# Kernel optimization log

Hardware: AMD Instinct MI355X
Metric: run time of the kernel (lower is better)

## Reference

```python
import jax, jax.numpy as jnp
import numpy as np

B, T, D = 1, 2048, 2048
HQ, HKV = 32, 8
DH = D // HQ          # 64
NREP = HQ // HKV      # 4


def _apply_rope(x, cos, sin):
    # x: (B, T, H, DH); cos/sin: (T, DH//2). Complex multiply on interleaved pairs:
    # (x0 + i*x1) * (c + i*s) -> (x0*c - x1*s, x0*s + x1*c)
    b, t, h, d = x.shape
    xr = x.reshape(b, t, h, d // 2, 2)
    x0, x1 = xr[..., 0], xr[..., 1]
    c = cos[:t][None, :, None, :]
    s = sin[:t][None, :, None, :]
    o0 = x0 * c - x1 * s
    o1 = x0 * s + x1 * c
    return jnp.stack([o0, o1], axis=-1).reshape(b, t, h, d)


def setup_inputs() -> dict:
    key = jax.random.key(0)
    ks = jax.random.split(key, 6)
    w = 0.02
    x = jax.random.normal(ks[0], (B, T, D), dtype=jnp.float32)
    Wq = jax.random.normal(ks[1], (HQ * DH, D), dtype=jnp.float32) * w
    Wk = jax.random.normal(ks[2], (HKV * DH, D), dtype=jnp.float32) * w
    Wv = jax.random.normal(ks[3], (HKV * DH, D), dtype=jnp.float32) * w
    Wo = jax.random.normal(ks[4], (D, HQ * DH), dtype=jnp.float32) * w
    # standard RoPE frequencies, theta = 10000
    inv_freq = 1.0 / (10000.0 ** (np.arange(0, DH, 2, dtype=np.float32) / DH))
    angles = np.arange(T, dtype=np.float32)[:, None] * inv_freq[None, :]  # (T, DH//2)
    rope_cos = jnp.asarray(np.cos(angles))
    rope_sin = jnp.asarray(np.sin(angles))
    mask = jnp.tril(jnp.ones((T, T), dtype=bool))  # causal
    return {"x": x, "Wq": Wq, "Wk": Wk, "Wv": Wv, "Wo": Wo,
            "rope_cos": rope_cos, "rope_sin": rope_sin, "mask": mask}


def reference(x, Wq, Wk, Wv, Wo, rope_cos, rope_sin, mask):
    b, t, d = x.shape
    q = (x @ Wq.T).reshape(b, t, HQ, DH)
    k = (x @ Wk.T).reshape(b, t, HKV, DH)
    v = (x @ Wv.T).reshape(b, t, HKV, DH)
    q = _apply_rope(q, rope_cos, rope_sin)
    k = _apply_rope(k, rope_cos, rope_sin)
    # GQA: head index = kv_head * NREP + rep (matches torch expand+reshape order)
    qg = q.reshape(b, t, HKV, NREP, DH)
    scale = jnp.sqrt(jnp.float32(DH))
    # scores: (B, HKV, NREP, T, S) without materializing expanded K
    scores = jnp.einsum('bthrd,bshd->bhrts', qg, k) / scale
    scores = jnp.where(mask[None, None, None, :t, :t], scores, -jnp.inf)
    attn = jax.nn.softmax(scores, axis=-1)
    out = jnp.einsum('bhrts,bshd->bthrd', attn, v)  # (B, T, HKV, NREP, DH)
    out = out.reshape(b, t, HQ * DH)
    return out @ Wo.T
```

## Files before the change

kernel.cpp:

```cpp
#include <hip/hip_runtime.h>
#include <math.h>
#include <stdint.h>

static constexpr int T   = 2048;
static constexpr int D   = 2048;
static constexpr int HQ  = 32;
static constexpr int HKV = 8;
static constexpr int DH  = 64;
static constexpr int DKV = HKV * DH;
static constexpr int NQKV = D + 2 * DKV;

typedef float f32x4 __attribute__((ext_vector_type(4)));
typedef __bf16 bf16x8 __attribute__((ext_vector_type(8)));
typedef __bf16 bf16x2 __attribute__((ext_vector_type(2)));
typedef unsigned short u16x8 __attribute__((ext_vector_type(8)));
typedef unsigned short u16x4 __attribute__((ext_vector_type(4)));

__device__ __forceinline__ unsigned short f2bf(float f) {
  union { float f; unsigned u; } v; v.f = f;
  unsigned u = v.u;
  return (unsigned short)((u + 0x7FFFu + ((u >> 16) & 1u)) >> 16);
}
__device__ __forceinline__ float bf2f(unsigned short b) {
  union { unsigned u; float f; } v; v.u = ((unsigned)b) << 16;
  return v.f;
}
__device__ __forceinline__ unsigned pk2bf(float a, float b) {
#if __has_builtin(__builtin_amdgcn_cvt_pk_bf16_f32)
  bf16x2 r = __builtin_amdgcn_cvt_pk_bf16_f32(a, b);
  return __builtin_bit_cast(unsigned, r);
#else
  return (unsigned)f2bf(a) | ((unsigned)f2bf(b) << 16);
#endif
}
__device__ __forceinline__ float fexp2(float x) {
#if __has_builtin(__builtin_amdgcn_exp2f)
  return __builtin_amdgcn_exp2f(x);
#else
  return exp2f(x);
#endif
}
__device__ __forceinline__ float frcp(float x) {
#if __has_builtin(__builtin_amdgcn_rcpf)
  return __builtin_amdgcn_rcpf(x);
#else
  return 1.0f / x;
#endif
}
__device__ __forceinline__ f32x4 mfma16(u16x8 a, u16x8 b, f32x4 c) {
  return __builtin_amdgcn_mfma_f32_16x16x32_bf16(
      __builtin_bit_cast(bf16x8, a), __builtin_bit_cast(bf16x8, b), c, 0, 0, 0);
}
__device__ __forceinline__ void gld16(const unsigned short* g, unsigned short* l) {
  __builtin_amdgcn_global_load_lds(
      (const __attribute__((address_space(1))) unsigned*)g,
      (__attribute__((address_space(3))) unsigned*)l, 16, 0, 0);
}

__global__ __launch_bounds__(256) void cvt_all(const float* __restrict__ x,
                                               const float* __restrict__ Wq,
                                               const float* __restrict__ Wk,
                                               const float* __restrict__ Wv,
                                               const float* __restrict__ Wo,
                                               unsigned short* __restrict__ xb,
                                               unsigned short* __restrict__ wqkv,
                                               unsigned short* __restrict__ wob) {
  int b = blockIdx.x;
  const float* src;
  unsigned short* dst;
  if (b < 2048)      { src = x;  dst = xb; }
  else if (b < 4096) { src = Wq; dst = wqkv;                          b -= 2048; }
  else if (b < 4608) { src = Wk; dst = wqkv + (size_t)D * D;          b -= 4096; }
  else if (b < 5120) { src = Wv; dst = wqkv + (size_t)(D + DKV) * D;  b -= 4608; }
  else               { src = Wo; dst = wob;                           b -= 5120; }
  size_t i = ((size_t)b * 256 + threadIdx.x) * 8;
  float4 a = *(const float4*)(src + i);
  float4 c = *(const float4*)(src + i + 4);
  uint4 r = {pk2bf(a.x, a.y), pk2bf(a.z, a.w), pk2bf(c.x, c.y), pk2bf(c.z, c.w)};
  *(uint4*)(dst + i) = r;
}

template <bool OUT_BF16>
__global__ __launch_bounds__(256) void gemm_bt_bf16(const unsigned short* __restrict__ A,
                                                    const unsigned short* __restrict__ Bt,
                                                    void* __restrict__ Cv,
                                                    int N, int K) {
  __shared__ alignas(16) unsigned short As[64 * 128];
  __shared__ alignas(16) unsigned short Bs[128 * 128];

  const int bn = blockIdx.x * 128, bm = blockIdx.y * 64;
  const int tid = threadIdx.x, w = tid >> 6, lane = tid & 63;
  const int c = lane & 15, quad = lane >> 4;

  const int r4 = lane >> 4, ch = lane & 15;
  const unsigned short* aRow = A + (size_t)(bm + w * 16 + r4) * K;
  const unsigned short* bRow = Bt + (size_t)(bn + w * 32 + r4) * K;
  unsigned short* AsW = As + (w * 16) * 128;
  unsigned short* BsW = Bs + (w * 32) * 128;

  f32x4 acc[4][2] = {};

  for (int k0 = 0; k0 < K; k0 += 128) {
#pragma unroll
    for (int j = 0; j < 4; j++) {
      const int sch = ch ^ ((j * 4 + r4) & 15);
      gld16(aRow + (size_t)(j * 4) * K + k0 + sch * 8, AsW + j * 4 * 128);
    }
#pragma unroll
    for (int j = 0; j < 8; j++) {
      const int sch = ch ^ ((j * 4 + r4) & 15);
      gld16(bRow + (size_t)(j * 4) * K + k0 + sch * 8, BsW + j * 4 * 128);
    }
    __syncthreads();

#pragma unroll
    for (int ks = 0; ks < 4; ks++) {
      const int slot = (ks * 4 + quad) ^ c;
      u16x8 a[4], b[2];
#pragma unroll
      for (int mi = 0; mi < 4; mi++)
        a[mi] = *(const u16x8*)&As[(mi * 16 + c) * 128 + slot * 8];
#pragma unroll
      for (int ni = 0; ni < 2; ni++)
        b[ni] = *(const u16x8*)&Bs[(w * 32 + ni * 16 + c) * 128 + slot * 8];
#pragma unroll
      for (int mi = 0; mi < 4; mi++)
#pragma unroll
        for (int ni = 0; ni < 2; ni++)
          acc[mi][ni] = mfma16(a[mi], b[ni], acc[mi][ni]);
    }
    __syncthreads();
  }

#pragma unroll
  for (int mi = 0; mi < 4; mi++)
#pragma unroll
    for (int ni = 0; ni < 2; ni++)
#pragma unroll
      for (int r = 0; r < 4; r++) {
        size_t row = (size_t)(bm + mi * 16 + quad * 4 + r);
        size_t col = (size_t)(bn + w * 32 + ni * 16 + c);
        if (OUT_BF16)
          ((unsigned short*)Cv)[row * N + col] = f2bf(acc[mi][ni][r]);
        else
          ((float*)Cv)[row * N + col] = acc[mi][ni][r];
      }
}

__global__ __launch_bounds__(256) void rope_tv(unsigned short* __restrict__ QKV,
                                               const float* __restrict__ cosb,
                                               const float* __restrict__ sinb,
                                               unsigned short* __restrict__ VT) {
  const int QP = T * HQ * (DH / 2);
  if (blockIdx.x < 10240) {
    int idx = blockIdx.x * 256 + threadIdx.x;
    unsigned short* p;
    int t, i;
    float sc;
    if (idx < QP) {
      t = idx / (HQ * DH / 2);
      int rem = idx - t * (HQ * DH / 2);
      i = rem & 31;
      p = QKV + (size_t)t * NQKV + rem * 2;
      sc = 0.125f * 1.44269504088896340736f;
    } else {
      int j = idx - QP;
      t = j / (HKV * DH / 2);
      int rem = j - t * (HKV * DH / 2);
      i = rem & 31;
      p = QKV + (size_t)t * NQKV + D + rem * 2;
      sc = 1.0f;
    }
    float x0 = bf2f(p[0]), x1 = bf2f(p[1]);
    float cs = cosb[t * 32 + i], sn = sinb[t * 32 + i];
    *(unsigned*)p = pk2bf((x0 * cs - x1 * sn) * sc, (x0 * sn + x1 * cs) * sc);
  } else {
    __shared__ unsigned short Ts[64][65];
    const int bid = blockIdx.x - 10240;
    const int tb = bid & 31, db = bid >> 5;
    const int tid = threadIdx.x;
    const int r = tid >> 2, c0 = (tid & 3) * 16;
    const unsigned short* src = QKV + (size_t)(tb * 64 + r) * NQKV + (D + DKV) + db * 64 + c0;
    *(u16x8*)&Ts[r][c0]     = *(const u16x8*)src;
    *(u16x8*)&Ts[r][c0 + 8] = *(const u16x8*)(src + 8);
    __syncthreads();
    u16x8 a, b;
#pragma unroll
    for (int j = 0; j < 8; j++) a[j] = Ts[c0 + j][r];
#pragma unroll
    for (int j = 0; j < 8; j++) b[j] = Ts[c0 + 8 + j][r];
    unsigned short* dst = VT + (size_t)(db * 64 + r) * T + tb * 64 + c0;
    *(u16x8*)dst = a;
    *(u16x8*)(dst + 8) = b;
  }
}

__global__ __launch_bounds__(256) void attn_kernel(const unsigned short* __restrict__ QKV,
                                                   const unsigned short* __restrict__ VT,
                                                   unsigned short* __restrict__ Ob) {
  const int kh = blockIdx.x;
  const int NQT = T / 16;
  const int tid = threadIdx.x, w = tid >> 6, lane = tid & 63;
  const int c = lane & 15, quad = lane >> 4;
  const int h = kh * 4 + w;

  __shared__ alignas(16) unsigned short Kt[64 * 64];
  __shared__ alignas(16) unsigned short Vt[64 * 64];
  __shared__ alignas(16) unsigned short Pb[4 * 16 * 72];

  unsigned short* PbW = Pb + w * 16 * 72;

  const int srow = lane >> 3;
  const int sch  = (lane & 7) ^ srow;
  const unsigned short* kgBase = QKV + D + (size_t)(w * 16 + srow) * NQKV + kh * DH + sch * 8;
  const unsigned short* vgBase = VT + (size_t)(kh * DH + w * 16 + srow) * T + sch * 8;
  unsigned short* KtW = Kt + (w * 16) * 64;
  unsigned short* VtW = Vt + (w * 16) * 64;

#pragma unroll 1
  for (int pass = 0; pass < 2; pass++) {
    const int qt = pass ? (NQT - 1 - (int)blockIdx.y) : (int)blockIdx.y;
    const int qbase = qt * 16;

    u16x8 qf[2];
    {
      const unsigned short* qp = QKV + (size_t)(qbase + c) * NQKV + h * DH + quad * 8;
      qf[0] = *(const u16x8*)qp;
      qf[1] = *(const u16x8*)(qp + 32);
    }

    f32x4 o[4] = {};
    float m = -INFINITY, l = 0.f;

    const int nFull = qt >> 2;
    for (int st = 0; st <= nFull; st++) {
      __syncthreads();
#pragma unroll
      for (int j = 0; j < 2; j++) {
        gld16(kgBase + ((size_t)st * 64 + (size_t)j * 8) * NQKV, KtW + j * 8 * 64);
        gld16(vgBase + (size_t)j * 8 * T + st * 64, VtW + j * 8 * 64);
      }
      __syncthreads();

      f32x4 sacc[4] = {};
#pragma unroll
      for (int ks = 0; ks < 2; ks++) {
#pragma unroll
        for (int ni = 0; ni < 4; ni++) {
          const int slot = (ks * 4 + quad) ^ (c & 7);
          u16x8 kf = *(const u16x8*)&Kt[(ni * 16 + c) * 64 + slot * 8];
          sacc[ni] = mfma16(kf, qf[ks], sacc[ni]);
        }
      }

      if (st == nFull) {
        const int qrow = qbase + c;
#pragma unroll
        for (int ni = 0; ni < 4; ni++)
#pragma unroll
          for (int r = 0; r < 4; r++) {
            int key = st * 64 + ni * 16 + quad * 4 + r;
            if (key > qrow) sacc[ni][r] = -INFINITY;
          }
      }

      float tmax = sacc[0][0];
#pragma unroll
      for (int ni = 0; ni < 4; ni++)
#pragma unroll
        for (int r = 0; r < 4; r++) tmax = fmaxf(tmax, sacc[ni][r]);
      tmax = fmaxf(tmax, __shfl_xor(tmax, 16, 64));
      tmax = fmaxf(tmax, __shfl_xor(tmax, 32, 64));
      float mnew = fmaxf(m, tmax);
      float alpha = fexp2(m - mnew);
      m = mnew;

      float psum = 0.f;
#pragma unroll
      for (int ni = 0; ni < 4; ni++) {
        float p0 = fexp2(sacc[ni][0] - mnew);
        float p1 = fexp2(sacc[ni][1] - mnew);
        float p2 = fexp2(sacc[ni][2] - mnew);
        float p3 = fexp2(sacc[ni][3] - mnew);
        psum += (p0 + p1) + (p2 + p3);
        uint2 pr = {pk2bf(p0, p1), pk2bf(p2, p3)};
        *(uint2*)&PbW[c * 72 + ni * 16 + quad * 4] = pr;
      }
      psum += __shfl_xor(psum, 16, 64);
      psum += __shfl_xor(psum, 32, 64);
      l = l * alpha + psum;

      float aR[4];
#pragma unroll
      for (int r = 0; r < 4; r++) aR[r] = __shfl(alpha, quad * 4 + r, 64);
#pragma unroll
      for (int ni = 0; ni < 4; ni++)
#pragma unroll
        for (int r = 0; r < 4; r++) o[ni][r] *= aR[r];

#pragma unroll
      for (int ks = 0; ks < 2; ks++) {
        u16x8 pf = *(const u16x8*)&PbW[c * 72 + ks * 32 + quad * 8];
#pragma unroll
        for (int ni = 0; ni < 4; ni++) {
          const int slot = (ks * 4 + quad) ^ (c & 7);
          u16x8 vf = *(const u16x8*)&Vt[(ni * 16 + c) * 64 + slot * 8];
          o[ni] = mfma16(pf, vf, o[ni]);
        }
      }
    }

    float lR[4];
#pragma unroll
    for (int r = 0; r < 4; r++) lR[r] = frcp(__shfl(l, quad * 4 + r, 64));
#pragma unroll
    for (int ni = 0; ni < 4; ni++)
#pragma unroll
      for (int r = 0; r < 4; r++) {
        size_t row = (size_t)(qbase + quad * 4 + r);
        size_t col = (size_t)(h * DH + ni * 16 + c);
        Ob[row * D + col] = f2bf(o[ni][r] * lR[r]);
      }
  }
}

extern "C" void kernel_launch(void* const* d_in, const int* in_sizes, int n_in,
                              void* d_out, int out_size, void* d_ws, size_t ws_size,
                              hipStream_t stream) {
  const float* x  = (const float*)d_in[0];
  const float* Wq = (const float*)d_in[1];
  const float* Wk = (const float*)d_in[2];
  const float* Wv = (const float*)d_in[3];
  const float* Wo = (const float*)d_in[4];
  const float* rc = (const float*)d_in[5];
  const float* rs = (const float*)d_in[6];
  float* out = (float*)d_out;

  char* ws = (char*)d_ws;
  unsigned short* xb   = (unsigned short*)(ws);
  unsigned short* wqkv = (unsigned short*)(ws + (size_t)(8u  << 20));
  unsigned short* wob  = (unsigned short*)(ws + (size_t)(20u << 20));
  unsigned short* qkvb = (unsigned short*)(ws + (size_t)(28u << 20));
  unsigned short* Ab   = xb;
  unsigned short* VT   = wqkv;

  cvt_all<<<dim3(7168), 256, 0, stream>>>(x, Wq, Wk, Wv, Wo, xb, wqkv, wob);

  gemm_bt_bf16<true><<<dim3(NQKV / 128, T / 64), 256, 0, stream>>>(xb, wqkv, qkvb, NQKV, D);

  rope_tv<<<dim3(10240 + 256), 256, 0, stream>>>(qkvb, rc, rs, VT);

  attn_kernel<<<dim3(HKV, T / 32), 256, 0, stream>>>(qkvb, VT, Ab);

  gemm_bt_bf16<false><<<dim3(D / 128, T / 64), 256, 0, stream>>>(Ab, wob, out, D, D);
}
```

Before: 228.3 us.

## Double-buffer GEMM and attention tiles, one query tile per attention block

The GEMM drops from one 128-wide K tile to two ping-pong 64-wide shared-memory buffers. The next tile's async global-to-LDS load is issued before computing on the current one, leaving one barrier per iteration. The attention kernel gets the same K/V double buffering. It also drops the paired forward/reverse query-tile passes in favour of one query tile per block, launched in reverse order to put the heavy tiles first. This aims to hide load latency and raise parallelism, but it loses the causal load pairing and adds LDS use.

After: 233.2 us. 2.1% more time.

```diff
diff --git a/kernel.cpp b/kernel.cpp
--- a/kernel.cpp
+++ b/kernel.cpp
@@ -85,51 +85,54 @@
                                                     const unsigned short* __restrict__ Bt,
                                                     void* __restrict__ Cv,
                                                     int N, int K) {
-  __shared__ alignas(16) unsigned short As[64 * 128];
-  __shared__ alignas(16) unsigned short Bs[128 * 128];
+  __shared__ alignas(16) unsigned short As[2][64 * 64];
+  __shared__ alignas(16) unsigned short Bs[2][128 * 64];
 
   const int bn = blockIdx.x * 128, bm = blockIdx.y * 64;
   const int tid = threadIdx.x, w = tid >> 6, lane = tid & 63;
   const int c = lane & 15, quad = lane >> 4;
 
-  const int r4 = lane >> 4, ch = lane & 15;
-  const unsigned short* aRow = A + (size_t)(bm + w * 16 + r4) * K;
-  const unsigned short* bRow = Bt + (size_t)(bn + w * 32 + r4) * K;
-  unsigned short* AsW = As + (w * 16) * 128;
-  unsigned short* BsW = Bs + (w * 32) * 128;
+  const int sr8 = lane >> 3;
+  const int sc8 = (lane & 7) ^ sr8;
+  const unsigned short* aRow = A + (size_t)(bm + w * 16 + sr8) * K + sc8 * 8;
+  const unsigned short* bRow = Bt + (size_t)(bn + w * 32 + sr8) * K + sc8 * 8;
 
   f32x4 acc[4][2] = {};
 
-  for (int k0 = 0; k0 < K; k0 += 128) {
-#pragma unroll
-    for (int j = 0; j < 4; j++) {
-      const int sch = ch ^ ((j * 4 + r4) & 15);
-      gld16(aRow + (size_t)(j * 4) * K + k0 + sch * 8, AsW + j * 4 * 128);
-    }
-#pragma unroll
-    for (int j = 0; j < 8; j++) {
-      const int sch = ch ^ ((j * 4 + r4) & 15);
-      gld16(bRow + (size_t)(j * 4) * K + k0 + sch * 8, BsW + j * 4 * 128);
-    }
+#pragma unroll
+  for (int j = 0; j < 2; j++)
+    gld16(aRow + (size_t)(j * 8) * K, &As[0][(w * 16 + j * 8) * 64]);
+#pragma unroll
+  for (int j = 0; j < 4; j++)
+    gld16(bRow + (size_t)(j * 8) * K, &Bs[0][(w * 32 + j * 8) * 64]);
+
+  for (int k0 = 0; k0 < K; k0 += 64) {
+    const int cur = (k0 >> 6) & 1;
     __syncthreads();
-
-#pragma unroll
-    for (int ks = 0; ks < 4; ks++) {
-      const int slot = (ks * 4 + quad) ^ c;
+    if (k0 + 64 < K) {
+#pragma unroll
+      for (int j = 0; j < 2; j++)
+        gld16(aRow + (size_t)(j * 8) * K + k0 + 64, &As[cur ^ 1][(w * 16 + j * 8) * 64]);
+#pragma unroll
+      for (int j = 0; j < 4; j++)
+        gld16(bRow + (size_t)(j * 8) * K + k0 + 64, &Bs[cur ^ 1][(w * 32 + j * 8) * 64]);
+    }
+#pragma unroll
+    for (int ks = 0; ks < 2; ks++) {
+      const int slot = (ks * 4 + quad) ^ (c & 7);
       u16x8 a[4], b[2];
 #pragma unroll
       for (int mi = 0; mi < 4; mi++)
-        a[mi] = *(const u16x8*)&As[(mi * 16 + c) * 128 + slot * 8];
+        a[mi] = *(const u16x8*)&As[cur][(mi * 16 + c) * 64 + slot * 8];
 #pragma unroll
       for (int ni = 0; ni < 2; ni++)
-        b[ni] = *(const u16x8*)&Bs[(w * 32 + ni * 16 + c) * 128 + slot * 8];
+        b[ni] = *(const u16x8*)&Bs[cur][(w * 32 + ni * 16 + c) * 64 + slot * 8];
 #pragma unroll
       for (int mi = 0; mi < 4; mi++)
 #pragma unroll
         for (int ni = 0; ni < 2; ni++)
           acc[mi][ni] = mfma16(a[mi], b[ni], acc[mi][ni]);
     }
-    __syncthreads();
   }
 
 #pragma unroll
@@ -199,129 +202,133 @@
                                                    const unsigned short* __restrict__ VT,
                                                    unsigned short* __restrict__ Ob) {
   const int kh = blockIdx.x;
-  const int NQT = T / 16;
+  const int qt = (int)(gridDim.y - 1 - blockIdx.y);
+  const int qbase = qt * 16;
   const int tid = threadIdx.x, w = tid >> 6, lane = tid & 63;
   const int c = lane & 15, quad = lane >> 4;
   const int h = kh * 4 + w;
 
-  __shared__ alignas(16) unsigned short Kt[64 * 64];
-  __shared__ alignas(16) unsigned short Vt[64 * 64];
+  __shared__ alignas(16) unsigned short Kt[2][64 * 64];
+  __shared__ alignas(16) unsigned short Vt[2][64 * 64];
   __shared__ alignas(16) unsigned short Pb[4 * 16 * 72];
 
   unsigned short* PbW = Pb + w * 16 * 72;
+
+  u16x8 qf[2];
+  {
+    const unsigned short* qp = QKV + (size_t)(qbase + c) * NQKV + h * DH + quad * 8;
+    qf[0] = *(const u16x8*)qp;
+    qf[1] = *(const u16x8*)(qp + 32);
+  }
 
   const int srow = lane >> 3;
   const int sch  = (lane & 7) ^ srow;
   const unsigned short* kgBase = QKV + D + (size_t)(w * 16 + srow) * NQKV + kh * DH + sch * 8;
   const unsigned short* vgBase = VT + (size_t)(kh * DH + w * 16 + srow) * T + sch * 8;
-  unsigned short* KtW = Kt + (w * 16) * 64;
-  unsigned short* VtW = Vt + (w * 16) * 64;
-
-#pragma unroll 1
-  for (int pass = 0; pass < 2; pass++) {
-    const int qt = pass ? (NQT - 1 - (int)blockIdx.y) : (int)blockIdx.y;
-    const int qbase = qt * 16;
-
-    u16x8 qf[2];
-    {
-      const unsigned short* qp = QKV + (size_t)(qbase + c) * NQKV + h * DH + quad * 8;
-      qf[0] = *(const u16x8*)qp;
-      qf[1] = *(const u16x8*)(qp + 32);
-    }
-
-    f32x4 o[4] = {};
-    float m = -INFINITY, l = 0.f;
-
-    const int nFull = qt >> 2;
-    for (int st = 0; st <= nFull; st++) {
-      __syncthreads();
+
+  f32x4 o[4] = {};
+  float m = -INFINITY, l = 0.f;
+
+  const int nFull = qt >> 2;
+
+#pragma unroll
+  for (int j = 0; j < 2; j++) {
+    gld16(kgBase + (size_t)(j * 8) * NQKV, &Kt[0][(w * 16 + j * 8) * 64]);
+    gld16(vgBase + (size_t)(j * 8) * T, &Vt[0][(w * 16 + j * 8) * 64]);
+  }
+
+  for (int st = 0; st <= nFull; st++) {
+    const int cur = st & 1;
+    __syncthreads();
+    if (st < nFull) {
 #pragma unroll
       for (int j = 0; j < 2; j++) {
-        gld16(kgBase + ((size_t)st * 64 + (size_t)j * 8) * NQKV, KtW + j * 8 * 64);
-        gld16(vgBase + (size_t)j * 8 * T + st * 64, VtW + j * 8 * 64);
+        gld16(kgBase + ((size_t)(st + 1) * 64 + (size_t)j * 8) * NQKV,
+              &Kt[cur ^ 1][(w * 16 + j * 8) * 64]);
+        gld16(vgBase + (size_t)(j * 8) * T + (st + 1) * 64,
+              &Vt[cur ^ 1][(w * 16 + j * 8) * 64]);
       }
-      __syncthreads();
-
-      f32x4 sacc[4] = {};
-#pragma unroll
-      for (int ks = 0; ks < 2; ks++) {
-#pragma unroll
-        for (int ni = 0; ni < 4; ni++) {
-          const int slot = (ks * 4 + quad) ^ (c & 7);
-          u16x8 kf = *(const u16x8*)&Kt[(ni * 16 + c) * 64 + slot * 8];
-          sacc[ni] = mfma16(kf, qf[ks], sacc[ni]);
+    }
+
+    f32x4 sacc[4] = {};
+#pragma unroll
+    for (int ks = 0; ks < 2; ks++) {
+#pragma unroll
+      for (int ni = 0; ni < 4; ni++) {
+        const int slot = (ks * 4 + quad) ^ (c & 7);
+        u16x8 kf = *(const u16x8*)&Kt[cur][(ni * 16 + c) * 64 + slot * 8];
+        sacc[ni] = mfma16(kf, qf[ks], sacc[ni]);
+      }
+    }
+
+    if (st == nFull) {
+      const int qrow = qbase + c;
+#pragma unroll
+      for (int ni = 0; ni < 4; ni++)
+#pragma unroll
+        for (int r = 0; r < 4; r++) {
+          int key = st * 64 + ni * 16 + quad * 4 + r;
+          if (key > qrow) sacc[ni][r] = -INFINITY;
         }
+    }
+
+    float tmax = sacc[0][0];
+#pragma unroll
+    for (int ni = 0; ni < 4; ni++)
+#pragma unroll
+      for (int r = 0; r < 4; r++) tmax = fmaxf(tmax, sacc[ni][r]);
+    tmax = fmaxf(tmax, __shfl_xor(tmax, 16, 64));
+    tmax = fmaxf(tmax, __shfl_xor(tmax, 32, 64));
+    float mnew = fmaxf(m, tmax);
+    float alpha = fexp2(m - mnew);
+    m = mnew;
+
+    float psum = 0.f;
+#pragma unroll
+    for (int ni = 0; ni < 4; ni++) {
+      float p0 = fexp2(sacc[ni][0] - mnew);
+      float p1 = fexp2(sacc[ni][1] - mnew);
+      float p2 = fexp2(sacc[ni][2] - mnew);
+      float p3 = fexp2(sacc[ni][3] - mnew);
+      psum += (p0 + p1) + (p2 + p3);
+      uint2 pr = {pk2bf(p0, p1), pk2bf(p2, p3)};
+      *(uint2*)&PbW[c * 72 + ni * 16 + quad * 4] = pr;
+    }
+    psum += __shfl_xor(psum, 16, 64);
+    psum += __shfl_xor(psum, 32, 64);
+    l = l * alpha + psum;
+
+    float aR[4];
+#pragma unroll
+    for (int r = 0; r < 4; r++) aR[r] = __shfl(alpha, quad * 4 + r, 64);
+#pragma unroll
+    for (int ni = 0; ni < 4; ni++)
+#pragma unroll
+      for (int r = 0; r < 4; r++) o[ni][r] *= aR[r];
+
+#pragma unroll
+    for (int ks = 0; ks < 2; ks++) {
+      u16x8 pf = *(const u16x8*)&PbW[c * 72 + ks * 32 + quad * 8];
+#pragma unroll
+      for (int ni = 0; ni < 4; ni++) {
+        const int slot = (ks * 4 + quad) ^ (c & 7);
+        u16x8 vf = *(const u16x8*)&Vt[cur][(ni * 16 + c) * 64 + slot * 8];
+        o[ni] = mfma16(pf, vf, o[ni]);
       }
-
-      if (st == nFull) {
-        const int qrow = qbase + c;
-#pragma unroll
-        for (int ni = 0; ni < 4; ni++)
-#pragma unroll
-          for (int r = 0; r < 4; r++) {
-            int key = st * 64 + ni * 16 + quad * 4 + r;
-            if (key > qrow) sacc[ni][r] = -INFINITY;
-          }
-      }
-
-      float tmax = sacc[0][0];
-#pragma unroll
-      for (int ni = 0; ni < 4; ni++)
-#pragma unroll
-        for (int r = 0; r < 4; r++) tmax = fmaxf(tmax, sacc[ni][r]);
-      tmax = fmaxf(tmax, __shfl_xor(tmax, 16, 64));
-      tmax = fmaxf(tmax, __shfl_xor(tmax, 32, 64));
-      float mnew = fmaxf(m, tmax);
-      float alpha = fexp2(m - mnew);
-      m = mnew;
-
-      float psum = 0.f;
-#pragma unroll
-      for (int ni = 0; ni < 4; ni++) {
-        float p0 = fexp2(sacc[ni][0] - mnew);
-        float p1 = fexp2(sacc[ni][1] - mnew);
-        float p2 = fexp2(sacc[ni][2] - mnew);
-        float p3 = fexp2(sacc[ni][3] - mnew);
-        psum += (p0 + p1) + (p2 + p3);
-        uint2 pr = {pk2bf(p0, p1), pk2bf(p2, p3)};
-        *(uint2*)&PbW[c * 72 + ni * 16 + quad * 4] = pr;
-      }
-      psum += __shfl_xor(psum, 16, 64);
-      psum += __shfl_xor(psum, 32, 64);
-      l = l * alpha + psum;
-
-      float aR[4];
-#pragma unroll
-      for (int r = 0; r < 4; r++) aR[r] = __shfl(alpha, quad * 4 + r, 64);
-#pragma unroll
-      for (int ni = 0; ni < 4; ni++)
-#pragma unroll
-        for (int r = 0; r < 4; r++) o[ni][r] *= aR[r];
-
-#pragma unroll
-      for (int ks = 0; ks < 2; ks++) {
-        u16x8 pf = *(const u16x8*)&PbW[c * 72 + ks * 32 + quad * 8];
-#pragma unroll
-        for (int ni = 0; ni < 4; ni++) {
-          const int slot = (ks * 4 + quad) ^ (c & 7);
-          u16x8 vf = *(const u16x8*)&Vt[(ni * 16 + c) * 64 + slot * 8];
-          o[ni] = mfma16(pf, vf, o[ni]);
-        }
-      }
-    }
-
-    float lR[4];
-#pragma unroll
-    for (int r = 0; r < 4; r++) lR[r] = frcp(__shfl(l, quad * 4 + r, 64));
-#pragma unroll
-    for (int ni = 0; ni < 4; ni++)
-#pragma unroll
-      for (int r = 0; r < 4; r++) {
-        size_t row = (size_t)(qbase + quad * 4 + r);
-        size_t col = (size_t)(h * DH + ni * 16 + c);
-        Ob[row * D + col] = f2bf(o[ni][r] * lR[r]);
-      }
-  }
+    }
+  }
+
+  float lR[4];
+#pragma unroll
+  for (int r = 0; r < 4; r++) lR[r] = frcp(__shfl(l, quad * 4 + r, 64));
+#pragma unroll
+  for (int ni = 0; ni < 4; ni++)
+#pragma unroll
+    for (int r = 0; r < 4; r++) {
+      size_t row = (size_t)(qbase + quad * 4 + r);
+      size_t col = (size_t)(h * DH + ni * 16 + c);
+      Ob[row * D + col] = f2bf(o[ni][r] * lR[r]);
+    }
 }
 
 extern "C" void kernel_launch(void* const* d_in, const int* in_sizes, int n_in,
@@ -350,7 +357,7 @@
 
   rope_tv<<<dim3(10240 + 256), 256, 0, stream>>>(qkvb, rc, rs, VT);
 
-  attn_kernel<<<dim3(HKV, T / 32), 256, 0, stream>>>(qkvb, VT, Ab);
+  attn_kernel<<<dim3(HKV, T / 16), 256, 0, stream>>>(qkvb, VT, Ab);
 
   gemm_bt_bf16<false><<<dim3(D / 128, T / 64), 256, 0, stream>>>(Ab, wob, out, D, D);
 }
```
